# Optimization experiments

Hardware: AMD Instinct MI355X
Metric: run time of the kernel (lower is better)

## Reference

```python
import jax, jax.numpy as jnp
import numpy as np

N = 8192
QS = 128
KS = 128
F = 256
EPS = 1e-5     # BatchNorm1d default eps
SLOPE = 0.01   # LeakyReLU default negative_slope


def _leaky(x):
    return jnp.where(x >= 0, x, SLOPE * x)


def _mlp_bn(x, w1, b1, w2, b2, gamma, beta):
    # Sequential(Linear, LeakyReLU, Linear, LeakyReLU) then BatchNorm1d (training mode)
    h = _leaky(x @ w1 + b1)
    h = _leaky(h @ w2 + b2)
    mean = h.mean(axis=0)
    var = h.var(axis=0)  # biased variance, as torch BN uses for normalization
    return gamma * (h - mean) * jax.lax.rsqrt(var + EPS) + beta


def setup_inputs() -> dict:
    key = jax.random.key(0)
    ks = jax.random.split(key, 24)

    def lin_w(k_, fi, fo):
        s = 1.0 / np.sqrt(fi)
        return jax.random.uniform(k_, (fi, fo), minval=-s, maxval=s, dtype=jnp.float32)

    def lin_b(k_, fi, fo):
        s = 1.0 / np.sqrt(fi)
        return jax.random.uniform(k_, (fo,), minval=-s, maxval=s, dtype=jnp.float32)

    A = (jax.random.uniform(ks[0], (N, N)) < 0.004).astype(jnp.float32)
    q = jax.random.normal(ks[1], (N, QS), dtype=jnp.float32)
    k = jax.random.normal(ks[2], (N, KS), dtype=jnp.float32)

    inp = {"A": A, "q": q, "k": k}
    i = 3
    for pre, fi in (("q", QS), ("k", KS), ("v", KS)):
        inp[pre + "_w1"] = lin_w(ks[i], fi, F); i += 1
        inp[pre + "_b1"] = lin_b(ks[i], fi, F); i += 1
        inp[pre + "_w2"] = lin_w(ks[i], F, F); i += 1
        inp[pre + "_b2"] = lin_b(ks[i], F, F); i += 1
        inp[pre + "_gamma"] = jnp.ones((F,), jnp.float32)
        inp[pre + "_beta"] = jnp.zeros((F,), jnp.float32)
    return inp


def reference(A, q, k,
              q_w1, q_b1, q_w2, q_b2, q_gamma, q_beta,
              k_w1, k_b1, k_w2, k_b2, k_gamma, k_beta,
              v_w1, v_b1, v_w2, v_b2, v_gamma, v_beta):
    qe1 = _mlp_bn(q, q_w1, q_b1, q_w2, q_b2, q_gamma, q_beta)   # [N, F]
    ke1 = _mlp_bn(k, k_w1, k_b1, k_w2, k_b2, k_gamma, k_beta)   # [N, F]
    prod = (qe1 @ ke1.T) / jnp.sqrt(jnp.float32(F))             # [N, N]
    # NOTE: faithful to source — mask zeroes scores (not -inf) before softmax
    masked = A * prod
    attn = jax.nn.softmax(masked, axis=1)
    ve1 = _mlp_bn(k, v_w1, v_b1, v_w2, v_b2, v_gamma, v_beta)   # [N, F]
    return attn @ ve1                                            # [N, F]
```

## Files before the change

### kernel.cpp

```cpp
#include <hip/hip_runtime.h>

#define NROWS 8192
#define FDIM 256
#define CAP 128

typedef _Float16 half8_t __attribute__((ext_vector_type(8)));
typedef _Float16 half4_t __attribute__((ext_vector_type(4)));
typedef float floatx4 __attribute__((ext_vector_type(4)));

struct MlpPtrs {
  const float* w1[3]; const float* b1[3];
  const float* w2[3]; const float* b2[3];
  const float* gamma[3]; const float* beta[3];
};

__device__ __forceinline__ void scan_row(
    int r, int lane, int wave, const float* __restrict__ A,
    int* __restrict__ colidx, int* __restrict__ rowcnt,
    int (*sj)[CAP], int* cnt) {
  if (lane == 0) cnt[wave] = 0;
  const floatx4* row = (const floatx4*)(A + (size_t)r * NROWS);
  floatx4 av[32];
  #pragma unroll
  for (int it = 0; it < 32; ++it)
    av[it] = __builtin_nontemporal_load(&row[it * 64 + lane]);
  #pragma unroll
  for (int it = 0; it < 32; ++it) {
    int base = (it * 64 + lane) * 4;
    int cols[4]; int c = 0;
    if (av[it][0] != 0.f) cols[c++] = base + 0;
    if (av[it][1] != 0.f) cols[c++] = base + 1;
    if (av[it][2] != 0.f) cols[c++] = base + 2;
    if (av[it][3] != 0.f) cols[c++] = base + 3;
    if (c) {
      int pos = atomicAdd(&cnt[wave], c);
      for (int l = 0; l < c; ++l) if (pos + l < CAP) sj[wave][pos + l] = cols[l];
    }
  }
  int nnz = cnt[wave] < CAP ? cnt[wave] : CAP;
  if (lane < nnz) colidx[(size_t)r * CAP + lane] = sj[wave][lane];
  if (lane + 64 < nnz) colidx[(size_t)r * CAP + lane + 64] = sj[wave][lane + 64];
  if (lane == 0) rowcnt[r] = nnz;
}

__global__ __launch_bounds__(256) void prep_kernel(
    MlpPtrs p, _Float16* __restrict__ w1p, _Float16* __restrict__ w2p) {
  int task = blockIdx.y;
  int tid = blockIdx.x * 256 + threadIdx.x;
  int m = task % 3;
  bool isw2 = task >= 3;
  int K = isw2 ? 256 : 128;
  if (tid >= K * 256) return;
  const float* src = isw2 ? p.w2[m] : p.w1[m];
  _Float16* dst = isw2 ? (w2p + m * 65536) : (w1p + m * 32768);
  int j = tid & 7, lane = (tid >> 3) & 63, rest = tid >> 9;
  int ktiles = K >> 5;
  int k_tile = rest % ktiles, n_tile = rest / ktiles;
  int kk = k_tile * 32 + (lane >> 4) * 8 + j;
  int nn = n_tile * 16 + (lane & 15);
  dst[tid] = (_Float16)src[kk * 256 + nn];
}

__global__ __launch_bounds__(256) void mlp_kernel(
    const float* __restrict__ q, const float* __restrict__ k,
    const _Float16* __restrict__ w1p, const _Float16* __restrict__ w2p, MlpPtrs p,
    _Float16* __restrict__ e1, float* __restrict__ colsum, float* __restrict__ colsumsq,
    const float* __restrict__ A, int* __restrict__ colidx, int* __restrict__ rowcnt) {
  __shared__ __align__(16) char smraw[64 * 264 * 2];
  int lane = threadIdx.x & 63, wave = threadIdx.x >> 6;
  int bid = blockIdx.x;
  if (bid < 2048) {
    int (*sj)[CAP] = (int (*)[CAP])smraw;
    int* cnt = (int*)(smraw + sizeof(int) * 4 * CAP);
    scan_row(bid * 4 + wave, lane, wave, A, colidx, rowcnt, sj, cnt);
    return;
  }
  _Float16 (*hT)[264] = (_Float16 (*)[264])smraw;
  int t = bid - 2048;
  int z = t % 3, bx = t / 3;
  int m0 = bx * 64;
  const float* X = (z == 0) ? q : k;
  const half8_t* w1p8 = (const half8_t*)(w1p + z * 32768);
  const half8_t* w2p8 = (const half8_t*)(w2p + z * 65536);
  int lm = lane & 15, lq = lane >> 4;

  floatx4 acc[4][4];
  #pragma unroll
  for (int a = 0; a < 4; ++a)
    #pragma unroll
    for (int b = 0; b < 4; ++b) acc[a][b] = (floatx4){0.f, 0.f, 0.f, 0.f};

  const float* xp = X + (size_t)(m0 + lm) * 128 + lq * 8;
  #pragma unroll
  for (int kt = 0; kt < 4; ++kt) {
    half8_t xf[4];
    #pragma unroll
    for (int rr = 0; rr < 4; ++rr) {
      floatx4 a0 = *(const floatx4*)(xp + rr * 16 * 128 + kt * 32);
      floatx4 a1 = *(const floatx4*)(xp + rr * 16 * 128 + kt * 32 + 4);
      xf[rr] = (half8_t){(_Float16)a0[0], (_Float16)a0[1], (_Float16)a0[2], (_Float16)a0[3],
                         (_Float16)a1[0], (_Float16)a1[1], (_Float16)a1[2], (_Float16)a1[3]};
    }
    #pragma unroll
    for (int u = 0; u < 4; ++u) {
      half8_t wf = w1p8[((wave * 4 + u) * 4 + kt) * 64 + lane];
      #pragma unroll
      for (int rr = 0; rr < 4; ++rr)
        acc[rr][u] = __builtin_amdgcn_mfma_f32_16x16x32_f16(wf, xf[rr], acc[rr][u], 0, 0, 0);
    }
  }
  {
    const float* b1 = p.b1[z];
    #pragma unroll
    for (int u = 0; u < 4; ++u) {
      floatx4 bb = *(const floatx4*)(b1 + (wave * 4 + u) * 16 + lq * 4);
      #pragma unroll
      for (int rr = 0; rr < 4; ++rr) {
        half4_t hv;
        #pragma unroll
        for (int r = 0; r < 4; ++r) {
          float v = acc[rr][u][r] + bb[r];
          v = (v >= 0.f) ? v : 0.01f * v;
          hv[r] = (_Float16)v;
        }
        *(half4_t*)(&hT[rr * 16 + lm][(wave * 4 + u) * 16 + lq * 4]) = hv;
      }
    }
  }
  __syncthreads();

  #pragma unroll
  for (int a = 0; a < 4; ++a)
    #pragma unroll
    for (int b = 0; b < 4; ++b) acc[a][b] = (floatx4){0.f, 0.f, 0.f, 0.f};
  #pragma unroll
  for (int kt = 0; kt < 8; ++kt) {
    half8_t af[4];
    #pragma unroll
    for (int rr = 0; rr < 4; ++rr)
      af[rr] = *(const half8_t*)(&hT[rr * 16 + lm][kt * 32 + lq * 8]);
    #pragma unroll
    for (int u = 0; u < 4; ++u) {
      half8_t bf = w2p8[((wave * 4 + u) * 8 + kt) * 64 + lane];
      #pragma unroll
      for (int rr = 0; rr < 4; ++rr)
        acc[rr][u] = __builtin_amdgcn_mfma_f32_16x16x32_f16(af[rr], bf, acc[rr][u], 0, 0, 0);
    }
  }
  const float* b2 = p.b2[z];
  _Float16* out = e1 + (size_t)z * (NROWS * FDIM);
  #pragma unroll
  for (int u = 0; u < 4; ++u) {
    int col = wave * 64 + u * 16 + lm;
    float bb = b2[col];
    float s = 0.f, s2 = 0.f;
    #pragma unroll
    for (int rr = 0; rr < 4; ++rr) {
      #pragma unroll
      for (int r = 0; r < 4; ++r) {
        float v = acc[rr][u][r] + bb;
        v = (v >= 0.f) ? v : 0.01f * v;
        out[(size_t)(m0 + rr * 16 + lq * 4 + r) * FDIM + col] = (_Float16)v;
        s += v; s2 += v * v;
      }
    }
    s  += __shfl_xor(s, 16, 64);  s  += __shfl_xor(s, 32, 64);
    s2 += __shfl_xor(s2, 16, 64); s2 += __shfl_xor(s2, 32, 64);
    if (lq == 0) {
      atomicAdd(&colsum[z * FDIM + col], s);
      atomicAdd(&colsumsq[z * FDIM + col], s2);
    }
  }
}

__global__ __launch_bounds__(256) void attn_kernel(
    const int* __restrict__ colidx, const int* __restrict__ rowcnt,
    const _Float16* __restrict__ e1,
    const float* __restrict__ colsum, const float* __restrict__ colsumsq,
    MlpPtrs p, float* __restrict__ out) {
  const _Float16* qe = e1;
  const _Float16* ke = e1 + (size_t)1 * NROWS * FDIM;
  const _Float16* ve = e1 + (size_t)2 * NROWS * FDIM;
  int lane = threadIdx.x & 63, wave = threadIdx.x >> 6;
  int i = blockIdx.x * 4 + wave;
  __shared__ int sj[4][CAP];
  __shared__ float sw[4][CAP];
  __shared__ __align__(16) float sscale[3 * FDIM];
  __shared__ __align__(16) float sshift[3 * FDIM];

  {
    int c = threadIdx.x;
    #pragma unroll
    for (int m = 0; m < 3; ++m) {
      float mean = colsum[m * FDIM + c] * (1.f / NROWS);
      float var = colsumsq[m * FDIM + c] * (1.f / NROWS) - mean * mean;
      float sc = p.gamma[m][c] * rsqrtf(var + 1e-5f);
      sscale[m * FDIM + c] = sc;
      sshift[m * FDIM + c] = p.beta[m][c] - mean * sc;
    }
  }
  int nnz = rowcnt[i];
  if (lane < nnz) sj[wave][lane] = colidx[(size_t)i * CAP + lane];
  if (lane + 64 < nnz) sj[wave][lane + 64] = colidx[(size_t)i * CAP + lane + 64];
  __syncthreads();

  int cl = lane & 15, g = lane >> 4;
  const half8_t* qp = (const half8_t*)(qe + (size_t)i * FDIM + cl * 16);
  half8_t qa = qp[0], qb8 = qp[1];
  const floatx4* sq4 = (const floatx4*)(sscale + cl * 16);
  const floatx4* hq4 = (const floatx4*)(sshift + cl * 16);
  const floatx4* sk4 = (const floatx4*)(sscale + FDIM + cl * 16);
  const floatx4* hk4 = (const floatx4*)(sshift + FDIM + cl * 16);
  float qk[16]; float qb = 0.f;
  #pragma unroll
  for (int v4 = 0; v4 < 4; ++v4) {
    floatx4 sq = sq4[v4], hq = hq4[v4], sk = sk4[v4], hk = hk4[v4];
    #pragma unroll
    for (int r = 0; r < 4; ++r) {
      int c = v4 * 4 + r;
      float qr = (c < 8) ? (float)qa[c] : (float)qb8[c - 8];
      float qn = qr * sq[r] + hq[r];
      qk[c] = qn * sk[r] * 0.0625f;
      qb += qn * hk[r] * 0.0625f;
    }
  }

  for (int e = g; e < nnz; e += 4) {
    int j = sj[wave][e];
    const half8_t* kp = (const half8_t*)(ke + (size_t)j * FDIM + cl * 16);
    half8_t ka = kp[0], kb = kp[1];
    float s = qb;
    #pragma unroll
    for (int r = 0; r < 8; ++r)
      s += qk[r] * (float)ka[r] + qk[r + 8] * (float)kb[r];
    #pragma unroll
    for (int off = 8; off >= 1; off >>= 1) s += __shfl_xor(s, off, 64);
    if (cl == 0) sw[wave][e] = s;
  }

  float v0 = lane < nnz ? sw[wave][lane] : 0.f;
  float v1 = lane + 64 < nnz ? sw[wave][lane + 64] : 0.f;
  float m = fmaxf(fmaxf(v0, v1), 0.f);
  #pragma unroll
  for (int off = 32; off >= 1; off >>= 1) m = fmaxf(m, __shfl_xor(m, off, 64));
  float em = __expf(-m);
  float w0 = lane < nnz ? __expf(v0 - m) : 0.f;
  float w1 = lane + 64 < nnz ? __expf(v1 - m) : 0.f;
  float ls = w0 + w1;
  #pragma unroll
  for (int off = 32; off >= 1; off >>= 1) ls += __shfl_xor(ls, off, 64);
  if (lane < nnz) sw[wave][lane] = w0 - em;
  if (lane + 64 < nnz) sw[wave][lane + 64] = w1 - em;
  float wsum = ls - (float)nnz * em;
  float inv = 1.f / (ls + (float)(NROWS - nnz) * em);

  floatx4 acc = (floatx4){0.f, 0.f, 0.f, 0.f};
  for (int e = 0; e < nnz; ++e) {
    int j = sj[wave][e];
    float w = sw[wave][e];
    half4_t vv = *(const half4_t*)(ve + (size_t)j * FDIM + lane * 4);
    acc[0] += w * (float)vv[0]; acc[1] += w * (float)vv[1];
    acc[2] += w * (float)vv[2]; acc[3] += w * (float)vv[3];
  }

  floatx4 sv = *(const floatx4*)(sscale + 2 * FDIM + lane * 4);
  floatx4 sh = *(const floatx4*)(sshift + 2 * FDIM + lane * 4);
  floatx4 cs = *(const floatx4*)(colsum + 2 * FDIM + lane * 4);
  float bg = wsum + em * (float)NROWS;
  floatx4 o;
  #pragma unroll
  for (int r = 0; r < 4; ++r)
    o[r] = inv * (sv[r] * (acc[r] + em * cs[r]) + sh[r] * bg);
  __builtin_nontemporal_store(o, (floatx4*)(out + (size_t)i * FDIM + lane * 4));
}

extern "C" void kernel_launch(void* const* d_in, const int* in_sizes, int n_in,
                              void* d_out, int out_size, void* d_ws, size_t ws_size,
                              hipStream_t stream) {
  const float* A = (const float*)d_in[0];
  const float* q = (const float*)d_in[1];
  const float* k = (const float*)d_in[2];
  MlpPtrs p;
  for (int m = 0; m < 3; ++m) {
    const int b = 3 + m * 6;
    p.w1[m]    = (const float*)d_in[b + 0];
    p.b1[m]    = (const float*)d_in[b + 1];
    p.w2[m]    = (const float*)d_in[b + 2];
    p.b2[m]    = (const float*)d_in[b + 3];
    p.gamma[m] = (const float*)d_in[b + 4];
    p.beta[m]  = (const float*)d_in[b + 5];
  }
  char* ws = (char*)d_ws;
  const size_t MB = 1024 * 1024;
  _Float16* e1  = (_Float16*)(ws + 0);
  _Float16* w1p = (_Float16*)(ws + 12 * MB);
  _Float16* w2p = (_Float16*)(ws + 12 * MB + 512 * 1024);
  float* colsum   = (float*)(ws + 13 * MB);
  float* colsumsq = colsum + 3 * FDIM;
  int* colidx = (int*)(ws + 14 * MB);
  int* rowcnt = (int*)(ws + 18 * MB);

  (void)hipMemsetAsync(colsum, 0, 2 * 3 * FDIM * sizeof(float), stream);
  prep_kernel<<<dim3(256, 6, 1), 256, 0, stream>>>(p, w1p, w2p);
  mlp_kernel<<<2048 + 384, 256, 0, stream>>>(q, k, w1p, w2p, p, e1, colsum, colsumsq,
                                             A, colidx, rowcnt);
  attn_kernel<<<NROWS / 4, 256, 0, stream>>>(colidx, rowcnt, e1, colsum, colsumsq, p,
                                             (float*)d_out);
}
```

Before: 426.7 us.

## Fold colsum clear into prep, reorder mlp blocks, unroll attention gathers

Clears the column-sum buffer inside prep_kernel instead of issuing a separate memset, which removes one launch. mlp_kernel now schedules the 384 MLP blocks ahead of the 2048 adjacency-scan blocks so the compute blocks dispatch first. In the attention kernel, the score loop handles two neighbours per iteration, and the V gather uses 16-byte half8 loads with the two wave halves covering different edges, combined by a cross-half shuffle. These raise memory-level parallelism in the gathers at the cost of more registers and extra shuffles.

```diff
diff --git a/kernel.cpp b/kernel.cpp
--- a/kernel.cpp
+++ b/kernel.cpp
@@ -44,9 +44,11 @@
 }
 
 __global__ __launch_bounds__(256) void prep_kernel(
-    MlpPtrs p, _Float16* __restrict__ w1p, _Float16* __restrict__ w2p) {
+    MlpPtrs p, _Float16* __restrict__ w1p, _Float16* __restrict__ w2p,
+    float* __restrict__ colsum) {
   int task = blockIdx.y;
   int tid = blockIdx.x * 256 + threadIdx.x;
+  if (task == 0 && tid < 1536) colsum[tid] = 0.f;
   int m = task % 3;
   bool isw2 = task >= 3;
   int K = isw2 ? 256 : 128;
@@ -69,14 +71,14 @@
   __shared__ __align__(16) char smraw[64 * 264 * 2];
   int lane = threadIdx.x & 63, wave = threadIdx.x >> 6;
   int bid = blockIdx.x;
-  if (bid < 2048) {
+  if (bid >= 384) {
     int (*sj)[CAP] = (int (*)[CAP])smraw;
     int* cnt = (int*)(smraw + sizeof(int) * 4 * CAP);
-    scan_row(bid * 4 + wave, lane, wave, A, colidx, rowcnt, sj, cnt);
+    scan_row((bid - 384) * 4 + wave, lane, wave, A, colidx, rowcnt, sj, cnt);
     return;
   }
   _Float16 (*hT)[264] = (_Float16 (*)[264])smraw;
-  int t = bid - 2048;
+  int t = bid;
   int z = t % 3, bx = t / 3;
   int m0 = bx * 64;
   const float* X = (z == 0) ? q : k;
@@ -225,17 +227,29 @@
     }
   }
 
-  for (int e = g; e < nnz; e += 4) {
-    int j = sj[wave][e];
-    const half8_t* kp = (const half8_t*)(ke + (size_t)j * FDIM + cl * 16);
-    half8_t ka = kp[0], kb = kp[1];
-    float s = qb;
-    #pragma unroll
-    for (int r = 0; r < 8; ++r)
-      s += qk[r] * (float)ka[r] + qk[r + 8] * (float)kb[r];
-    #pragma unroll
-    for (int off = 8; off >= 1; off >>= 1) s += __shfl_xor(s, off, 64);
-    if (cl == 0) sw[wave][e] = s;
+  for (int e = g; e < nnz; e += 8) {
+    int j0 = sj[wave][e];
+    bool has1 = (e + 4) < nnz;
+    int j1 = sj[wave][has1 ? e + 4 : e];
+    const half8_t* kp0 = (const half8_t*)(ke + (size_t)j0 * FDIM + cl * 16);
+    const half8_t* kp1 = (const half8_t*)(ke + (size_t)j1 * FDIM + cl * 16);
+    half8_t ka0 = kp0[0], kb0 = kp0[1];
+    half8_t ka1 = kp1[0], kb1 = kp1[1];
+    float s0 = qb, s1 = qb;
+    #pragma unroll
+    for (int r = 0; r < 8; ++r) {
+      s0 += qk[r] * (float)ka0[r] + qk[r + 8] * (float)kb0[r];
+      s1 += qk[r] * (float)ka1[r] + qk[r + 8] * (float)kb1[r];
+    }
+    #pragma unroll
+    for (int off = 8; off >= 1; off >>= 1) {
+      s0 += __shfl_xor(s0, off, 64);
+      s1 += __shfl_xor(s1, off, 64);
+    }
+    if (cl == 0) {
+      sw[wave][e] = s0;
+      if (has1) sw[wave][e + 4] = s1;
+    }
   }
 
   float v0 = lane < nnz ? sw[wave][lane] : 0.f;
@@ -254,24 +268,36 @@
   float wsum = ls - (float)nnz * em;
   float inv = 1.f / (ls + (float)(NROWS - nnz) * em);
 
-  floatx4 acc = (floatx4){0.f, 0.f, 0.f, 0.f};
-  for (int e = 0; e < nnz; ++e) {
-    int j = sj[wave][e];
-    float w = sw[wave][e];
-    half4_t vv = *(const half4_t*)(ve + (size_t)j * FDIM + lane * 4);
-    acc[0] += w * (float)vv[0]; acc[1] += w * (float)vv[1];
-    acc[2] += w * (float)vv[2]; acc[3] += w * (float)vv[3];
-  }
-
-  floatx4 sv = *(const floatx4*)(sscale + 2 * FDIM + lane * 4);
-  floatx4 sh = *(const floatx4*)(sshift + 2 * FDIM + lane * 4);
-  floatx4 cs = *(const floatx4*)(colsum + 2 * FDIM + lane * 4);
+  int eh = lane >> 5, cl5 = lane & 31;
+  float acc8[8];
+  #pragma unroll
+  for (int r = 0; r < 8; ++r) acc8[r] = 0.f;
+  for (int e = 0; e < nnz; e += 4) {
+    int ee0 = e + eh, ee1 = e + 2 + eh;
+    int jj0 = sj[wave][ee0 < nnz ? ee0 : e];
+    int jj1 = sj[wave][ee1 < nnz ? ee1 : e];
+    float ww0 = ee0 < nnz ? sw[wave][ee0] : 0.f;
+    float ww1 = ee1 < nnz ? sw[wave][ee1] : 0.f;
+    half8_t va = *(const half8_t*)(ve + (size_t)jj0 * FDIM + cl5 * 8);
+    half8_t vb = *(const half8_t*)(ve + (size_t)jj1 * FDIM + cl5 * 8);
+    #pragma unroll
+    for (int r = 0; r < 8; ++r) acc8[r] += ww0 * (float)va[r];
+    #pragma unroll
+    for (int r = 0; r < 8; ++r) acc8[r] += ww1 * (float)vb[r];
+  }
+  #pragma unroll
+  for (int r = 0; r < 8; ++r) acc8[r] += __shfl_xor(acc8[r], 32, 64);
+
+  int cb = cl5 * 8 + eh * 4;
+  floatx4 sv = *(const floatx4*)(sscale + 2 * FDIM + cb);
+  floatx4 sh = *(const floatx4*)(sshift + 2 * FDIM + cb);
+  floatx4 cs = *(const floatx4*)(colsum + 2 * FDIM + cb);
   float bg = wsum + em * (float)NROWS;
   floatx4 o;
   #pragma unroll
   for (int r = 0; r < 4; ++r)
-    o[r] = inv * (sv[r] * (acc[r] + em * cs[r]) + sh[r] * bg);
-  __builtin_nontemporal_store(o, (floatx4*)(out + (size_t)i * FDIM + lane * 4));
+    o[r] = inv * (sv[r] * (acc8[eh * 4 + r] + em * cs[r]) + sh[r] * bg);
+  __builtin_nontemporal_store(o, (floatx4*)(out + (size_t)i * FDIM + cb));
 }
 
 extern "C" void kernel_launch(void* const* d_in, const int* in_sizes, int n_in,
@@ -300,9 +326,8 @@
   int* colidx = (int*)(ws + 14 * MB);
   int* rowcnt = (int*)(ws + 18 * MB);
 
-  (void)hipMemsetAsync(colsum, 0, 2 * 3 * FDIM * sizeof(float), stream);
-  prep_kernel<<<dim3(256, 6, 1), 256, 0, stream>>>(p, w1p, w2p);
-  mlp_kernel<<<2048 + 384, 256, 0, stream>>>(q, k, w1p, w2p, p, e1, colsum, colsumsq,
+  prep_kernel<<<dim3(256, 6, 1), 256, 0, stream>>>(p, w1p, w2p, colsum);
+  mlp_kernel<<<384 + 2048, 256, 0, stream>>>(q, k, w1p, w2p, p, e1, colsum, colsumsq,
                                              A, colidx, rowcnt);
   attn_kernel<<<NROWS / 4, 256, 0, stream>>>(colidx, rowcnt, e1, colsum, colsumsq, p,
                                              (float*)d_out);
```

Result: no change. 424.6 us (-0.5%).
